# Performance work log

Hardware: AMD Instinct MI355X
Metric: run time of the kernel (lower is better)

The kernel has to match this reference:

```python
import jax, jax.numpy as jnp
import numpy as np

T = 20.0          # logit temperature self.t
THRESH = 1.0      # self.threshold
D = 768
N_OBJ = 8
N_FRAMES = 5
N_ARGS = 3


def l2norm(x, axis):
    # F.normalize: x / max(||x||_2, eps)
    n = jnp.sqrt(jnp.sum(x * x, axis=axis, keepdims=True))
    return x / jnp.maximum(n, 1e-12)


def ce(logits, labels):
    # nn.CrossEntropyLoss / F.cross_entropy with mean reduction
    ls = jax.nn.log_softmax(logits, axis=-1)
    return -jnp.take_along_axis(ls, labels[:, None], axis=1).mean()


def setup_inputs() -> dict:
    key = jax.random.key(0)
    k1, k2, k3, k4 = jax.random.split(key, 4)
    B, C = 256, 504
    return {
        "obj_feat": jax.random.normal(k1, (B, N_FRAMES, N_OBJ, D), dtype=jnp.float32),
        "text_feature": jax.random.normal(k2, (B, N_FRAMES, 4, D), dtype=jnp.float32),
        "mdl_preds": jax.random.normal(k3, (B, N_FRAMES, C), dtype=jnp.float32),
        "label_tensor": jax.random.randint(k4, (B, N_FRAMES), 0, C, dtype=jnp.int64),
    }


def reference(obj_feat, text_feature, mdl_preds, label_tensor):
    B = text_feature.shape[0]
    NB = N_FRAMES * B  # 5B rows

    # ---- LossB: verb cross entropy over flattened first two dims ----
    C = mdl_preds.shape[-1]
    loss_v = ce(mdl_preds.reshape(NB, C), label_tensor.reshape(NB))

    # ---- normalize features along feature dim ----
    obj = l2norm(obj_feat, axis=3)                     # [B,5,8,768]
    txt = l2norm(text_feature, axis=3)                 # [B,5,4,768]

    obj_flat = obj.reshape(N_OBJ * NB, D)              # [40B,768]
    # args = text slots {0,2,3}
    arg = jnp.concatenate([txt[:, :, 0:1, :], txt[:, :, 2:, :]], axis=2).reshape(-1, D)  # [15B,768]

    logits = (arg @ obj_flat.T) * T                    # [15B,40B]
    logits4 = logits.reshape(NB, N_ARGS, NB, N_OBJ)
    max_value = logits4.max(axis=3)                    # [5B,3,5B]
    max_indices = logits4.argmax(axis=3)               # [5B,3,5B]

    # labels[i*3+j] = argmax over own objects + i*8
    diag_idx = jnp.diagonal(max_indices, axis1=0, axis2=2).T   # [5B,3]
    row = jnp.arange(NB)
    labels_wpg = (diag_idx + (row[:, None] << 3)).reshape(-1)  # [15B]
    loss_wpg = ce(logits.reshape(N_ARGS * NB, N_OBJ * NB), labels_wpg)

    # eye-mask tricks == take the diagonal over (row, candidate-video) axes
    mask = jnp.diagonal(max_value, axis1=0, axis2=2).T > THRESH  # [5B,3] bool
    midx = diag_idx                                              # [5B,3]

    arg3 = arg.reshape(NB, N_ARGS, D)
    txt4 = txt.reshape(NB, 4, D)
    maskf = mask.astype(arg3.dtype)[..., None]
    te = (arg3 * maskf).sum(axis=1) + txt4[:, 1, :]              # [5B,768]

    obj3 = obj_flat.reshape(NB, N_OBJ, D)
    gathered = jnp.take_along_axis(obj3, midx[..., None], axis=1)  # [5B,3,768]
    ve = (gathered * maskf).sum(axis=1)                            # [5B,768]

    te = l2norm(te, axis=1)
    ve = l2norm(ve, axis=1)
    logits_ec = (te @ ve.T) * T                                   # [5B,5B]
    lbl = jnp.arange(NB)
    loss_ec = 0.5 * (ce(logits_ec, lbl) + ce(logits_ec.T, lbl))

    return loss_wpg * 0.3 + loss_v * 0.2 + loss_ec * 0.5
```

## Files before the change

kernel.cpp:

```cpp
#include <hip/hip_runtime.h>
#include <hip/hip_bf16.h>
#include <cstdint>
#include <cstddef>

#define DD 768
#define TSCALE 20.0f

typedef short bf16x8 __attribute__((ext_vector_type(8)));
typedef float f32x4 __attribute__((ext_vector_type(4)));
typedef int   i32x4 __attribute__((ext_vector_type(4)));

__device__ inline float wsum(float v){
  #pragma unroll
  for (int m = 1; m < 64; m <<= 1) v += __shfl_xor(v, m, 64);
  return v;
}
__device__ inline float wmax(float v){
  #pragma unroll
  for (int m = 1; m < 64; m <<= 1) v = fmaxf(v, __shfl_xor(v, m, 64));
  return v;
}

__device__ inline void gload_lds16(const void* g, void* l){
  __builtin_amdgcn_global_load_lds(
      (const __attribute__((address_space(1))) uint32_t*)g,
      (__attribute__((address_space(3))) uint32_t*)l, 16, 0, 0);
}

__device__ inline void store_bf16x4(__hip_bfloat16* p, float4 x){
  __hip_bfloat16 t[4] = {__float2bfloat16(x.x), __float2bfloat16(x.y),
                         __float2bfloat16(x.z), __float2bfloat16(x.w)};
  *(ushort4*)p = *(const ushort4*)t;
}

__device__ inline void store_i8x4(int8_t* p, float4 x){
  int q0 = __float2int_rn(x.x * 127.f), q1 = __float2int_rn(x.y * 127.f);
  int q2 = __float2int_rn(x.z * 127.f), q3 = __float2int_rn(x.w * 127.f);
  uint32_t w = (uint32_t)(uint8_t)(int8_t)q0 | ((uint32_t)(uint8_t)(int8_t)q1 << 8) |
               ((uint32_t)(uint8_t)(int8_t)q2 << 16) | ((uint32_t)(uint8_t)(int8_t)q3 << 24);
  *(uint32_t*)p = w;
}

__global__ __launch_bounds__(512, 2) void diag_teve(
    const float* __restrict__ obj, const float* __restrict__ txt,
    const float* __restrict__ mdl, const int* __restrict__ lab,
    float* __restrict__ diagmax,
    int8_t* __restrict__ obji8, int8_t* __restrict__ argi8,
    __hip_bfloat16* __restrict__ tenb, __hip_bfloat16* __restrict__ venb,
    float* __restrict__ lossv_arr, float* __restrict__ zr, int C)
{
  __shared__ float so[8][DD];
  __shared__ float sa[3][DD];
  __shared__ float st1[DD];
  __shared__ float sdot[3][8];
  __shared__ float smask[3];
  __shared__ int   sbi[3];
  __shared__ float pmax[4], psum[4];

  const int i = blockIdx.x, tid = threadIdx.x;
  const int lane = tid & 63, w = tid >> 6;

  if (tid < 5) zr[i * 5 + tid] = 0.f;

  {
    const float* src = obj + ((size_t)i * 8 + w) * DD;
    float4 v[3]; float ss = 0.f;
    #pragma unroll
    for (int q = 0; q < 3; ++q){
      v[q] = ((const float4*)src)[lane + q * 64];
      ss += v[q].x * v[q].x + v[q].y * v[q].y + v[q].z * v[q].z + v[q].w * v[q].w;
    }
    ss = wsum(ss);
    float inv = 1.0f / fmaxf(sqrtf(ss), 1e-12f);
    #pragma unroll
    for (int q = 0; q < 3; ++q){
      float4 x = {v[q].x * inv, v[q].y * inv, v[q].z * inv, v[q].w * inv};
      ((float4*)&so[w][0])[lane + q * 64] = x;
      store_i8x4(obji8 + ((size_t)i * 8 + w) * DD + 4 * (lane + q * 64), x);
    }
  }

  if (w < 4){
    int s4 = (w == 0) ? 0 : ((w < 3) ? (w + 1) : 1);
    const float* ap = txt + ((size_t)i * 4 + s4) * DD;
    float4 a[3]; float ss = 0.f;
    #pragma unroll
    for (int q = 0; q < 3; ++q){
      a[q] = ((const float4*)ap)[lane + q * 64];
      ss += a[q].x * a[q].x + a[q].y * a[q].y + a[q].z * a[q].z + a[q].w * a[q].w;
    }
    ss = wsum(ss);
    float inv = 1.0f / fmaxf(sqrtf(ss), 1e-12f);
    #pragma unroll
    for (int q = 0; q < 3; ++q){
      a[q].x *= inv; a[q].y *= inv; a[q].z *= inv; a[q].w *= inv;
    }
    if (w < 3){
      #pragma unroll
      for (int q = 0; q < 3; ++q){
        ((float4*)&sa[w][0])[lane + q * 64] = a[q];
        store_i8x4(argi8 + (size_t)(i * 3 + w) * DD + 4 * (lane + q * 64), a[q]);
      }
    } else {
      #pragma unroll
      for (int q = 0; q < 3; ++q) ((float4*)st1)[lane + q * 64] = a[q];
    }
  } else {
    const int W = w - 4;
    const float* x = mdl + (size_t)i * C;
    float mx = -3.0e38f;
    for (int c = lane + W * 64; c < C; c += 256) mx = fmaxf(mx, x[c]);
    mx = wmax(mx);
    float s = 0.f;
    for (int c = lane + W * 64; c < C; c += 256) s += expf(x[c] - mx);
    s = wsum(s);
    if (lane == 0){ pmax[W] = mx; psum[W] = s; }
  }
  __syncthreads();

  {
    float4 v[3];
    #pragma unroll
    for (int q = 0; q < 3; ++q) v[q] = ((const float4*)&so[w][0])[lane + q * 64];
    #pragma unroll
    for (int j = 0; j < 3; ++j){
      float s = 0.f;
      #pragma unroll
      for (int q = 0; q < 3; ++q){
        float4 aq = ((const float4*)&sa[j][0])[lane + q * 64];
        s += aq.x * v[q].x + aq.y * v[q].y + aq.z * v[q].z + aq.w * v[q].w;
      }
      s = wsum(s);
      if (lane == 0) sdot[j][w] = s;
    }
    if (w == 3 && lane == 0){
      float M = fmaxf(fmaxf(pmax[0], pmax[1]), fmaxf(pmax[2], pmax[3]));
      float S = psum[0] * expf(pmax[0] - M) + psum[1] * expf(pmax[1] - M)
              + psum[2] * expf(pmax[2] - M) + psum[3] * expf(pmax[3] - M);
      lossv_arr[i] = logf(S) + M - mdl[(size_t)i * C + lab[i]];
    }
  }
  __syncthreads();

  if (w == 0 && lane < 3){
    float best = -3.0e38f; int bi = 0;
    #pragma unroll
    for (int k = 0; k < 8; ++k){
      float s = sdot[lane][k];
      if (s > best){ best = s; bi = k; }
    }
    float dm = best * TSCALE;
    diagmax[i * 3 + lane] = dm;
    smask[lane] = (dm > 1.0f) ? 1.0f : 0.0f;
    sbi[lane] = bi;
  }
  __syncthreads();

  if (w == 0){
    float m0 = smask[0], m1 = smask[1], m2 = smask[2];
    float4 te[3]; float ss = 0.f;
    #pragma unroll
    for (int q = 0; q < 3; ++q){
      float4 t1v = ((const float4*)st1)[lane + q * 64];
      float4 a0 = ((const float4*)&sa[0][0])[lane + q * 64];
      float4 a1 = ((const float4*)&sa[1][0])[lane + q * 64];
      float4 a2 = ((const float4*)&sa[2][0])[lane + q * 64];
      float4 t;
      t.x = ((t1v.x + m0 * a0.x) + m1 * a1.x) + m2 * a2.x;
      t.y = ((t1v.y + m0 * a0.y) + m1 * a1.y) + m2 * a2.y;
      t.z = ((t1v.z + m0 * a0.z) + m1 * a1.z) + m2 * a2.z;
      t.w = ((t1v.w + m0 * a0.w) + m1 * a1.w) + m2 * a2.w;
      te[q] = t;
      ss += t.x * t.x + t.y * t.y + t.z * t.z + t.w * t.w;
    }
    ss = wsum(ss);
    float inv = 1.0f / fmaxf(sqrtf(ss), 1e-12f);
    #pragma unroll
    for (int q = 0; q < 3; ++q){
      float4 x = {te[q].x * inv, te[q].y * inv, te[q].z * inv, te[q].w * inv};
      store_bf16x4(tenb + (size_t)i * DD + lane * 4 + q * 256, x);
    }
  } else if (w == 1){
    float m0 = smask[0], m1 = smask[1], m2 = smask[2];
    int b0 = sbi[0], b1 = sbi[1], b2 = sbi[2];
    float4 ve[3]; float ss = 0.f;
    #pragma unroll
    for (int q = 0; q < 3; ++q){
      float4 w0 = ((const float4*)&so[b0][0])[lane + q * 64];
      float4 w1 = ((const float4*)&so[b1][0])[lane + q * 64];
      float4 w2 = ((const float4*)&so[b2][0])[lane + q * 64];
      float4 t;
      t.x = ((m0 * w0.x + m1 * w1.x)) + m2 * w2.x;
      t.y = ((m0 * w0.y + m1 * w1.y)) + m2 * w2.y;
      t.z = ((m0 * w0.z + m1 * w1.z)) + m2 * w2.z;
      t.w = ((m0 * w0.w + m1 * w1.w)) + m2 * w2.w;
      ve[q] = t;
      ss += t.x * t.x + t.y * t.y + t.z * t.z + t.w * t.w;
    }
    ss = wsum(ss);
    float inv = 1.0f / fmaxf(sqrtf(ss), 1e-12f);
    #pragma unroll
    for (int q = 0; q < 3; ++q){
      float4 x = {ve[q].x * inv, ve[q].y * inv, ve[q].z * inv, ve[q].w * inv};
      store_bf16x4(venb + (size_t)i * DD + lane * 4 + q * 256, x);
    }
  }
}

#define MFMAI8(d, av, bv) d = __builtin_amdgcn_mfma_i32_16x16x64_i8(av, bv, d, 0, 0, 0)

__global__ __launch_bounds__(256, 3) void gemms_fused(
    const int8_t* __restrict__ A, const int8_t* __restrict__ B,
    float* __restrict__ sumexp,
    const __hip_bfloat16* __restrict__ ten, const __hip_bfloat16* __restrict__ ven,
    float* __restrict__ rowsum, float* __restrict__ colsum, float* __restrict__ Ldiag,
    int nec, int necx)
{
  __shared__ char lds[49152];
  const int tid = threadIdx.x;
  const int lane = tid & 63, wid = tid >> 6;

  if ((int)blockIdx.x < nec){
    const int bx = blockIdx.x % necx, by = blockIdx.x / necx;
    __hip_bfloat16* As = (__hip_bfloat16*)lds;
    __hip_bfloat16* Bs = (__hip_bfloat16*)(lds + 8192);
    char* AsB = lds; char* BsB = lds + 8192;
    const int wr = wid >> 1, wc = wid & 1;
    f32x4 acc[4][4];
    #pragma unroll
    for (int i2 = 0; i2 < 4; ++i2)
      #pragma unroll
      for (int j = 0; j < 4; ++j) acc[i2][j] = (f32x4){0.f, 0.f, 0.f, 0.f};
    const char* Ab = (const char*)(ten + (size_t)(by * 128) * DD);
    const char* Bb = (const char*)(ven + (size_t)(bx * 128) * DD);
    const int srow = tid >> 2, scol = (tid & 3) * 16;
    const int r = lane & 15, kg = (lane >> 4) * 8;

    for (int kb = 0; kb < DD * 2; kb += 64){
      gload_lds16(Ab + (size_t)srow * (DD*2) + kb + scol, AsB + tid * 16);
      gload_lds16(Ab + (size_t)(srow + 64) * (DD*2) + kb + scol, AsB + 4096 + tid * 16);
      gload_lds16(Bb + (size_t)srow * (DD*2) + kb + scol, BsB + tid * 16);
      gload_lds16(Bb + (size_t)(srow + 64) * (DD*2) + kb + scol, BsB + 4096 + tid * 16);
      __syncthreads();
      bf16x8 af[4], bfr[4];
      #pragma unroll
      for (int mi = 0; mi < 4; ++mi)
        af[mi] = *(const bf16x8*)&As[(wr * 64 + mi * 16 + r) * 32 + kg];
      #pragma unroll
      for (int ni = 0; ni < 4; ++ni)
        bfr[ni] = *(const bf16x8*)&Bs[(wc * 64 + ni * 16 + r) * 32 + kg];
      #pragma unroll
      for (int mi = 0; mi < 4; ++mi)
        #pragma unroll
        for (int ni = 0; ni < 4; ++ni)
          acc[mi][ni] = __builtin_amdgcn_mfma_f32_16x16x32_bf16(af[mi], bfr[ni], acc[mi][ni], 0, 0, 0);
      __syncthreads();
    }
    int rowbase = by * 128 + wr * 64 + ((lane >> 4) << 2);
    float colacc[4] = {0.f, 0.f, 0.f, 0.f};
    #pragma unroll
    for (int mi = 0; mi < 4; ++mi){
      #pragma unroll
      for (int rr = 0; rr < 4; ++rr){
        float s = 0.f;
        #pragma unroll
        for (int ni = 0; ni < 4; ++ni){
          float e = expf(fmaf(acc[mi][ni][rr], TSCALE, -TSCALE));
          s += e; colacc[ni] += e;
        }
        s += __shfl_xor(s, 1, 64); s += __shfl_xor(s, 2, 64);
        s += __shfl_xor(s, 4, 64); s += __shfl_xor(s, 8, 64);
        if ((lane & 15) == 0) atomicAdd(&rowsum[rowbase + mi * 16 + rr], s);
      }
    }
    #pragma unroll
    for (int ni = 0; ni < 4; ++ni){
      float c = colacc[ni];
      c += __shfl_xor(c, 16, 64); c += __shfl_xor(c, 32, 64);
      if (lane < 16) atomicAdd(&colsum[bx * 128 + wc * 64 + ni * 16 + lane], c);
    }
    if (bx == by){
      #pragma unroll
      for (int mi = 0; mi < 4; ++mi)
        #pragma unroll
        for (int ni = 0; ni < 4; ++ni)
          #pragma unroll
          for (int rr = 0; rr < 4; ++rr){
            int grow = wr * 64 + mi * 16 + ((lane >> 4) << 2) + rr;
            int gcol = wc * 64 + ni * 16 + (lane & 15);
            if (grow == gcol) Ldiag[by * 128 + grow] = acc[mi][ni][rr] * TSCALE;
          }
    }
    return;
  }

  const int wr = wid >> 1, wc = wid & 1;
  const int r = lane & 15, kg = lane >> 4;

  int g = blockIdx.x - nec;
  int bx = (g & 7) * 10 + (g >> 3) % 10;
  int by = (g >> 3) / 10;

  const int8_t* Abase = A + (size_t)by * 128 * DD;
  const int8_t* Bbase = B + (size_t)bx * 128 * DD;

  const int srow = tid >> 2, sc = tid & 3;
  const int ssw = ((sc ^ ((srow >> 1) & 3)) * 16);

  auto STAGE = [&](int p, int kt){
    gload_lds16(Abase + (size_t)srow * DD + kt * 64 + ssw, lds + p * 16384 + tid * 16);
    gload_lds16(Abase + (size_t)(64 + srow) * DD + kt * 64 + ssw, lds + p * 16384 + 4096 + tid * 16);
    gload_lds16(Bbase + (size_t)srow * DD + kt * 64 + ssw, lds + p * 16384 + 8192 + tid * 16);
    gload_lds16(Bbase + (size_t)(64 + srow) * DD + kt * 64 + ssw, lds + p * 16384 + 12288 + tid * 16);
  };
  auto LDA = [&](int p, int mi)->i32x4 {
    int row = wr * 64 + mi * 16 + r;
    return *(const i32x4*)(lds + p * 16384 + row * 64 + ((kg ^ ((row >> 1) & 3)) * 16));
  };
  auto LDB = [&](int p, int ni)->i32x4 {
    int row = wc * 64 + ni * 16 + r;
    return *(const i32x4*)(lds + p * 16384 + 8192 + row * 64 + ((kg ^ ((row >> 1) & 3)) * 16));
  };

  i32x4 acc[4][4];
  #pragma unroll
  for (int mi = 0; mi < 4; ++mi)
    #pragma unroll
    for (int ni = 0; ni < 4; ++ni) acc[mi][ni] = (i32x4){0, 0, 0, 0};

  STAGE(0, 0); STAGE(1, 1);
  #pragma unroll
  for (int t = 0; t < 12; ++t){
    if (t < 11) asm volatile("s_waitcnt vmcnt(4)" ::: "memory");
    else        asm volatile("s_waitcnt vmcnt(0)" ::: "memory");
    __builtin_amdgcn_s_barrier();
    __builtin_amdgcn_sched_barrier(0);
    if (t < 10) STAGE((t + 2) % 3, t + 2);
    const int p = t % 3;
    i32x4 af[4], bf[4];
    #pragma unroll
    for (int mi = 0; mi < 4; ++mi) af[mi] = LDA(p, mi);
    #pragma unroll
    for (int ni = 0; ni < 4; ++ni) bf[ni] = LDB(p, ni);
    __builtin_amdgcn_s_setprio(1);
    #pragma unroll
    for (int mi = 0; mi < 4; ++mi)
      #pragma unroll
      for (int ni = 0; ni < 4; ++ni) MFMAI8(acc[mi][ni], af[mi], bf[ni]);
    __builtin_amdgcn_s_setprio(0);
  }

  const float SC = TSCALE / 16129.0f;
  const int rowbase = by * 128 + wr * 64 + kg * 4;
  #pragma unroll
  for (int mi = 0; mi < 4; ++mi){
    #pragma unroll
    for (int rr = 0; rr < 4; ++rr){
      float s = 0.f;
      #pragma unroll
      for (int ni = 0; ni < 4; ++ni) s += expf(fmaf((float)acc[mi][ni][rr], SC, -TSCALE));
      s += __shfl_xor(s, 1, 64); s += __shfl_xor(s, 2, 64);
      s += __shfl_xor(s, 4, 64); s += __shfl_xor(s, 8, 64);
      if (r == 0) atomicAdd(&sumexp[rowbase + mi * 16 + rr], s);
    }
  }
}

__global__ __launch_bounds__(256) void finalize_kernel(
    const float* __restrict__ sumexp, const float* __restrict__ diagmax,
    const float* __restrict__ rowsum, const float* __restrict__ colsum,
    const float* __restrict__ Ldiag, const float* __restrict__ lossv_arr,
    float* __restrict__ out, int NB)
{
  int tid = threadIdx.x;
  float p = 0.f;
  for (int r = tid; r < 3 * NB; r += 256) p += logf(sumexp[r]) + TSCALE - diagmax[r];
  p *= (0.3f / (3.0f * NB));
  float q = 0.f, lv = 0.f;
  for (int i2 = tid; i2 < NB; i2 += 256){
    q += (logf(rowsum[i2]) + TSCALE - Ldiag[i2]) + (logf(colsum[i2]) + TSCALE - Ldiag[i2]);
    lv += lossv_arr[i2];
  }
  p += q * (0.25f / NB) + lv * (0.2f / NB);
  __shared__ float red[256];
  red[tid] = p; __syncthreads();
  for (int s = 128; s > 0; s >>= 1){ if (tid < s) red[tid] += red[tid + s]; __syncthreads(); }
  if (tid == 0) out[0] = red[0];
}

extern "C" void kernel_launch(void* const* d_in, const int* in_sizes, int n_in,
                              void* d_out, int out_size, void* d_ws, size_t ws_size,
                              hipStream_t stream) {
  const float* obj = (const float*)d_in[0];
  const float* txt = (const float*)d_in[1];
  const float* mdl = (const float*)d_in[2];
  const int*   lab = (const int*)d_in[3];

  const int NB = in_sizes[1] / (4 * DD);
  const int C  = in_sizes[2] / NB;

  float* ws = (float*)d_ws;
  size_t o = 0;
  int8_t* obji8 = (int8_t*)(ws + o); o += (size_t)NB * 8 * DD / 4;
  int8_t* argi8 = (int8_t*)(ws + o); o += (size_t)NB * 3 * DD / 4;
  __hip_bfloat16* tenb = (__hip_bfloat16*)(ws + o); o += (size_t)NB * DD / 2;
  __hip_bfloat16* venb = (__hip_bfloat16*)(ws + o); o += (size_t)NB * DD / 2;
  float* diagmax = ws + o; o += (size_t)3 * NB;
  float* Ldiag = ws + o; o += (size_t)NB;
  float* lossv_arr = ws + o; o += (size_t)NB;
  float* zr = ws + o;
  float* sumexp = zr;
  float* rowsum = zr + 3 * NB;
  float* colsum = rowsum + NB;

  diag_teve<<<NB, 512, 0, stream>>>(obj, txt, mdl, lab, diagmax, obji8, argi8,
                                    tenb, venb, lossv_arr, zr, C);
  const int necx = NB / 128;
  const int nec = necx * necx;
  const int nwpg = (NB * 3 / 128) * (NB * 8 / 128);
  gemms_fused<<<nec + nwpg, 256, 0, stream>>>(argi8, obji8, sumexp, tenb, venb,
                                              rowsum, colsum, Ldiag, nec, necx);
  finalize_kernel<<<1, 256, 0, stream>>>(sumexp, diagmax, rowsum, colsum, Ldiag, lossv_arr,
                                         (float*)d_out, NB);
}
```

Baseline: 102.1 us.

## Widen int8 WPG GEMM tile to 128x256 with double buffering

The int8 logits GEMM tile grows from 128x128 to 128x256 per block, so each wave computes a 64x128 sub-tile with 32 accumulators. This halves the number of WPG blocks and raises arithmetic intensity per LDS load. The triple-buffered pipeline with a partial vmcnt wait becomes double buffering with a full vmcnt(0) wait each step, and launch bounds drop from 3 to 2 blocks per CU. The trade is less latency hiding and lower occupancy in exchange for fewer blocks, less A-tile reloading and fewer atomics.

```diff
diff --git a/kernel.cpp b/kernel.cpp
--- a/kernel.cpp
+++ b/kernel.cpp
@@ -209,7 +209,7 @@
 
 #define MFMAI8(d, av, bv) d = __builtin_amdgcn_mfma_i32_16x16x64_i8(av, bv, d, 0, 0, 0)
 
-__global__ __launch_bounds__(256, 3) void gemms_fused(
+__global__ __launch_bounds__(256, 2) void gemms_fused(
     const int8_t* __restrict__ A, const int8_t* __restrict__ B,
     float* __restrict__ sumexp,
     const __hip_bfloat16* __restrict__ ten, const __hip_bfloat16* __restrict__ ven,
@@ -298,55 +298,63 @@
   const int r = lane & 15, kg = lane >> 4;
 
   int g = blockIdx.x - nec;
-  int bx = (g & 7) * 10 + (g >> 3) % 10;
-  int by = (g >> 3) / 10;
+  int bx = (g & 7) * 5 + (g >> 3) % 5;
+  int by = (g >> 3) / 5;
 
   const int8_t* Abase = A + (size_t)by * 128 * DD;
-  const int8_t* Bbase = B + (size_t)bx * 128 * DD;
-
-  const int srow = tid >> 2, sc = tid & 3;
-  const int ssw = ((sc ^ ((srow >> 1) & 3)) * 16);
+  const int8_t* Bbase = B + (size_t)bx * 256 * DD;
 
   auto STAGE = [&](int p, int kt){
-    gload_lds16(Abase + (size_t)srow * DD + kt * 64 + ssw, lds + p * 16384 + tid * 16);
-    gload_lds16(Abase + (size_t)(64 + srow) * DD + kt * 64 + ssw, lds + p * 16384 + 4096 + tid * 16);
-    gload_lds16(Bbase + (size_t)srow * DD + kt * 64 + ssw, lds + p * 16384 + 8192 + tid * 16);
-    gload_lds16(Bbase + (size_t)(64 + srow) * DD + kt * 64 + ssw, lds + p * 16384 + 12288 + tid * 16);
+    #pragma unroll
+    for (int j = 0; j < 2; ++j){
+      int c = j * 256 + tid;
+      int row = c >> 2, cc = c & 3;
+      int cc2 = cc ^ ((row >> 1) & 3);
+      gload_lds16(Abase + (size_t)row * DD + kt * 64 + cc2 * 16,
+                  lds + p * 24576 + c * 16);
+    }
+    #pragma unroll
+    for (int j = 0; j < 4; ++j){
+      int c = j * 256 + tid;
+      int row = c >> 2, cc = c & 3;
+      int cc2 = cc ^ ((row >> 1) & 3);
+      gload_lds16(Bbase + (size_t)row * DD + kt * 64 + cc2 * 16,
+                  lds + p * 24576 + 8192 + c * 16);
+    }
   };
   auto LDA = [&](int p, int mi)->i32x4 {
     int row = wr * 64 + mi * 16 + r;
-    return *(const i32x4*)(lds + p * 16384 + row * 64 + ((kg ^ ((row >> 1) & 3)) * 16));
+    return *(const i32x4*)(lds + p * 24576 + row * 64 + ((kg ^ ((row >> 1) & 3)) * 16));
   };
   auto LDB = [&](int p, int ni)->i32x4 {
-    int row = wc * 64 + ni * 16 + r;
-    return *(const i32x4*)(lds + p * 16384 + 8192 + row * 64 + ((kg ^ ((row >> 1) & 3)) * 16));
+    int row = wc * 128 + ni * 16 + r;
+    return *(const i32x4*)(lds + p * 24576 + 8192 + row * 64 + ((kg ^ ((row >> 1) & 3)) * 16));
   };
 
-  i32x4 acc[4][4];
+  i32x4 acc[4][8];
   #pragma unroll
   for (int mi = 0; mi < 4; ++mi)
     #pragma unroll
-    for (int ni = 0; ni < 4; ++ni) acc[mi][ni] = (i32x4){0, 0, 0, 0};
-
-  STAGE(0, 0); STAGE(1, 1);
+    for (int ni = 0; ni < 8; ++ni) acc[mi][ni] = (i32x4){0, 0, 0, 0};
+
+  STAGE(0, 0);
   #pragma unroll
   for (int t = 0; t < 12; ++t){
-    if (t < 11) asm volatile("s_waitcnt vmcnt(4)" ::: "memory");
-    else        asm volatile("s_waitcnt vmcnt(0)" ::: "memory");
+    asm volatile("s_waitcnt vmcnt(0)" ::: "memory");
     __builtin_amdgcn_s_barrier();
     __builtin_amdgcn_sched_barrier(0);
-    if (t < 10) STAGE((t + 2) % 3, t + 2);
-    const int p = t % 3;
-    i32x4 af[4], bf[4];
+    const int p = t & 1;
+    if (t < 11) STAGE(p ^ 1, t + 1);
+    i32x4 af[4], bf[8];
     #pragma unroll
     for (int mi = 0; mi < 4; ++mi) af[mi] = LDA(p, mi);
     #pragma unroll
-    for (int ni = 0; ni < 4; ++ni) bf[ni] = LDB(p, ni);
+    for (int ni = 0; ni < 8; ++ni) bf[ni] = LDB(p, ni);
     __builtin_amdgcn_s_setprio(1);
     #pragma unroll
     for (int mi = 0; mi < 4; ++mi)
       #pragma unroll
-      for (int ni = 0; ni < 4; ++ni) MFMAI8(acc[mi][ni], af[mi], bf[ni]);
+      for (int ni = 0; ni < 8; ++ni) MFMAI8(acc[mi][ni], af[mi], bf[ni]);
     __builtin_amdgcn_s_setprio(0);
   }
 
@@ -358,7 +366,7 @@
     for (int rr = 0; rr < 4; ++rr){
       float s = 0.f;
       #pragma unroll
-      for (int ni = 0; ni < 4; ++ni) s += expf(fmaf((float)acc[mi][ni][rr], SC, -TSCALE));
+      for (int ni = 0; ni < 8; ++ni) s += expf(fmaf((float)acc[mi][ni][rr], SC, -TSCALE));
       s += __shfl_xor(s, 1, 64); s += __shfl_xor(s, 2, 64);
       s += __shfl_xor(s, 4, 64); s += __shfl_xor(s, 8, 64);
       if (r == 0) atomicAdd(&sumexp[rowbase + mi * 16 + rr], s);
@@ -417,7 +425,7 @@
                                     tenb, venb, lossv_arr, zr, C);
   const int necx = NB / 128;
   const int nec = necx * necx;
-  const int nwpg = (NB * 3 / 128) * (NB * 8 / 128);
+  const int nwpg = (NB * 3 / 128) * (NB * 8 / 256);
   gemms_fused<<<nec + nwpg, 256, 0, stream>>>(argi8, obji8, sumexp, tenb, venb,
                                               rowsum, colsum, Ldiag, nec, necx);
   finalize_kernel<<<1, 256, 0, stream>>>(sumexp, diagmax, rowsum, colsum, Ldiag, lossv_arr,
```

New measurement: 90.42 us. 11.5% less time.
